# Optimization experiments

Hardware: AMD Instinct MI355X
Metric: run time of the kernel (lower is better)

The kernel has to match this reference:

```python
import jax, jax.numpy as jnp
import numpy as np

SIZES = (20, 20, 20, 20, 20)          # formula_oh_sizes
OH_N = sum(SIZES)                      # 100
NUM_BINS = 65536                       # spect_bin.get_num_bins()
EPS_SIZE = 1e-4                        # eps added to subset size
IN_EPS = 1e-5                          # torch InstanceNorm1d default eps


def thermometer_oh(counts):
    # StructuredOneHot with accum=True: per-element thermometer encoding.
    # counts: (N, E) element counts -> (N, sum(SIZES)) with out[j]=1 iff j < count.
    outs = [(jnp.arange(s, dtype=counts.dtype)[None, :] < counts[:, i:i + 1]).astype(jnp.float32)
            for i, s in enumerate(SIZES)]
    return jnp.concatenate(outs, axis=-1)


def inorm(x):
    # InstanceNorm1d (affine=False) as applied here: normalize over last dim per row.
    m = jnp.mean(x, axis=-1, keepdims=True)
    v = jnp.var(x, axis=-1, keepdims=True)
    return (x - m) * jax.lax.rsqrt(v + IN_EPS)


def _lin(key, fan_in, fan_out):
    k1, k2 = jax.random.split(key)
    bound = 1.0 / np.sqrt(fan_in)
    W = jax.random.uniform(k1, (fan_in, fan_out), jnp.float32, -bound, bound)
    b = jax.random.uniform(k2, (fan_out,), jnp.float32, -bound, bound)
    return W, b


def setup_inputs():
    key = jax.random.key(0)
    ks = jax.random.split(key, 12)
    B, A, GF, S, P, E, D = 8, 48, 256, 4096, 32, 5, 256
    vert_feat_in = jax.random.normal(ks[0], (B, A, GF), jnp.float32)
    vert_mask_in = jnp.ones((B, A), jnp.float32)
    elem_idx = jax.random.randint(ks[1], (B, A), 0, E)
    vert_element_oh = jax.nn.one_hot(elem_idx, E, dtype=jnp.float32)
    adj_oh = jnp.zeros((B, A, A), jnp.float32)                      # unused by forward path
    atom_subsets = jax.random.randint(ks[2], (B, S, A), 0, 2).astype(jnp.int32)
    atom_subsets_peaks = jnp.zeros((1,), jnp.float32)               # unused (mass_idx/intensity used)
    mass_idx = jax.random.randint(ks[3], (B, S, P), 0, NUM_BINS).astype(jnp.int32)
    intensity = jax.random.uniform(ks[4], (B, S, P), jnp.float32)
    combine_W, combine_b = _lin(ks[5], OH_N + GF, GF)
    l1_W, l1_b = _lin(ks[6], GF, D)
    l2a_W, l2a_b = _lin(ks[7], D, D)
    l2b_W, l2b_b = _lin(ks[8], D, D)
    score_W, score_b = _lin(ks[9], D, 1)
    return {
        'vert_feat_in': vert_feat_in, 'vert_mask_in': vert_mask_in,
        'vert_element_oh': vert_element_oh, 'adj_oh': adj_oh,
        'atom_subsets': atom_subsets, 'atom_subsets_peaks': atom_subsets_peaks,
        'mass_idx': mass_idx, 'intensity': intensity,
        'combine_W': combine_W, 'combine_b': combine_b,
        'l1_W': l1_W, 'l1_b': l1_b, 'l2a_W': l2a_W, 'l2a_b': l2a_b,
        'l2b_W': l2b_W, 'l2b_b': l2b_b, 'score_W': score_W, 'score_b': score_b,
    }


def reference(vert_feat_in, vert_mask_in, vert_element_oh, adj_oh, atom_subsets,
              atom_subsets_peaks, mass_idx, intensity,
              combine_W, combine_b, l1_W, l1_b, l2a_W, l2a_b, l2b_W, l2b_b,
              score_W, score_b):
    B, A, GF = vert_feat_in.shape
    _, S, _ = atom_subsets.shape
    subsets_f = atom_subsets.astype(jnp.float32)
    masked_vert = vert_feat_in * vert_mask_in[:, :, None]               # (B,A,GF)
    subsets_masked = subsets_f * vert_mask_in[:, None, :]               # (B,S,A)
    # weighted sum of vertex features over each subset
    sws = jnp.einsum('bag,bsa->bsg', masked_vert, subsets_masked)        # (B,S,GF)
    # per-subset element counts -> structured one-hot formula encoding
    counts = jnp.einsum('bae,bsa->bse', vert_element_oh, subsets_f)      # (B,S,E)
    pf_oh = thermometer_oh(counts.reshape(-1, counts.shape[-1])).reshape(B, S, OH_N)
    subset_size = jnp.sum(subsets_masked, axis=2) + EPS_SIZE             # (B,S)
    mean_feat = sws / subset_size[:, :, None]
    normed = inorm(mean_feat)                                            # subset_weighted_norm
    combined = jax.nn.relu(jnp.concatenate([pf_oh, normed], -1) @ combine_W + combine_b)
    x = inorm(combined)                                                  # norm_post_combine
    x = jax.nn.relu(x @ l1_W + l1_b)
    x = jax.nn.leaky_relu(x @ l2a_W + l2a_b)
    x = jax.nn.leaky_relu(x @ l2b_W + l2b_b)
    x = jax.nn.relu(x)
    x = inorm(x)                                                         # norm_pre_score
    scores = (x @ score_W + score_b)[..., 0]                             # (B,S)
    probs = jax.nn.softmax(scores, axis=-1)
    # per-batch sparse mass-matrix binning: scatter-add intensity*prob into spectral bins
    weighted = intensity * probs[:, :, None]                             # (B,S,P)
    seg = jax.vmap(lambda idx, w: jax.ops.segment_sum(w, idx, num_segments=NUM_BINS))
    spect_out = seg(mass_idx.reshape(B, -1), weighted.reshape(B, -1))    # (B,NUM_BINS)
    return spect_out, probs
```

## Files before the change

### kernel.cpp

```cpp
#include <hip/hip_runtime.h>
#include <math.h>

#define B_DIM 8
#define A_DIM 48
#define GF_DIM 256
#define S_DIM 4096
#define P_DIM 32
#define E_DIM 5
#define OHN 100
#define NBINS 65536
#define XF_STRIDE 268

typedef __attribute__((ext_vector_type(8))) short short8v;
typedef __attribute__((ext_vector_type(4))) float float4v;

__device__ __forceinline__ float wave_sum(float v) {
#pragma unroll
    for (int o = 32; o; o >>= 1) v += __shfl_xor(v, o, 64);
    return v;
}
__device__ __forceinline__ float wave_max(float v) {
#pragma unroll
    for (int o = 32; o; o >>= 1) v = fmaxf(v, __shfl_xor(v, o, 64));
    return v;
}
__device__ __forceinline__ float quad16_sum(float v) {
    v += __shfl_xor(v, 1, 64); v += __shfl_xor(v, 2, 64);
    v += __shfl_xor(v, 4, 64); v += __shfl_xor(v, 8, 64);
    return v;
}
__device__ __forceinline__ unsigned short bf16_rn(float x) {
    unsigned int u = __float_as_uint(x);
    return (unsigned short)((u + 0x7FFFu + ((u >> 16) & 1u)) >> 16);
}
__device__ __forceinline__ float bf16_val(unsigned short h) {
    return __uint_as_float(((unsigned int)h) << 16);
}

__global__ __launch_bounds__(256) void k_wprep(
    const float* __restrict__ cW, const float* __restrict__ l1W,
    const float* __restrict__ l2aW, const float* __restrict__ l2bW,
    short* __restrict__ wp)
{
    int e = blockIdx.x * 256 + threadIdx.x;
    int c = e >> 13;
    int i = e & 8191;
    int j    = i & 7;
    int lane = (i >> 3) & 63;
    int nt   = (i >> 9) & 1;
    int wn   = i >> 10;
    int krel = (lane >> 4) * 8 + j;
    int n    = wn * 32 + nt * 16 + (lane & 15);
    float val = 0.f;
    if (c < 12) {
        int kp = c * 32 + krel;
        if (kp < 100)       val = cW[kp * 256 + n];
        else if (kp >= 128) val = cW[(kp - 28) * 256 + n];
    } else {
        int L  = (c - 12) >> 3;
        int kc = (c - 12) & 7;
        const float* W = (L == 0) ? l1W : (L == 1) ? l2aW : l2bW;
        val = W[(kc * 32 + krel) * 256 + n];
    }
    unsigned short h = bf16_rn(val);
    float lo = val - bf16_val(h);
    int base = c * 16384 + (i & 511);
    wp[base + (wn * 4 + nt) * 512]     = (short)h;
    wp[base + (wn * 4 + 2 + nt) * 512] = (short)bf16_rn(lo);
}

__global__ __launch_bounds__(256) void k_features(
    const float* __restrict__ vert_feat, const float* __restrict__ vert_mask,
    const float* __restrict__ elem_oh, const int* __restrict__ subsets,
    float* __restrict__ x0)
{
    __shared__ float4 vertm[A_DIM][GF_DIM / 4];
    __shared__ float  maskL[A_DIM];
    __shared__ int    eiL[A_DIM];

    const int tid  = threadIdx.x;
    const int lane = tid & 63;
    const int w    = tid >> 6;
    const int b    = blockIdx.x >> 9;
    const int s0   = (blockIdx.x & 511) * 8;

    if (tid < A_DIM) {
        maskL[tid] = vert_mask[b * A_DIM + tid];
        int ei = 0;
#pragma unroll
        for (int e = 0; e < E_DIM; ++e)
            if (elem_oh[(b * A_DIM + tid) * E_DIM + e] > 0.5f) ei = e;
        eiL[tid] = ei;
    }
    __syncthreads();

    const float4* vb = (const float4*)(vert_feat + (size_t)b * A_DIM * GF_DIM);
    for (int idx = tid; idx < A_DIM * (GF_DIM / 4); idx += 256) {
        float4 v = vb[idx];
        float mk = maskL[idx >> 6];
        v.x *= mk; v.y *= mk; v.z *= mk; v.w *= mk;
        vertm[idx >> 6][idx & 63] = v;
    }
    __syncthreads();

    const int   myei   = (lane < A_DIM) ? eiL[lane] : -1;
    const float mymask = (lane < A_DIM) ? maskL[lane] : 0.0f;

#pragma unroll
    for (int i = 0; i < 2; ++i) {
        const int s = s0 + w * 2 + i;
        const int* fp = subsets + ((size_t)b * S_DIM + s) * A_DIM;
        int myflag = (lane < A_DIM) ? fp[lane] : 0;
        float fcoef = (float)myflag * mymask;

        float c0, c1, c2, c3, c4;
        {
            unsigned long long m0 = __ballot(myflag != 0 && myei == 0);
            unsigned long long m1 = __ballot(myflag != 0 && myei == 1);
            unsigned long long m2 = __ballot(myflag != 0 && myei == 2);
            unsigned long long m3 = __ballot(myflag != 0 && myei == 3);
            unsigned long long m4 = __ballot(myflag != 0 && myei == 4);
            c0 = (float)__popcll(m0); c1 = (float)__popcll(m1);
            c2 = (float)__popcll(m2); c3 = (float)__popcll(m3);
            c4 = (float)__popcll(m4);
        }
        float ssize = wave_sum(fcoef) + 1e-4f;

        float4 acc = make_float4(0.f, 0.f, 0.f, 0.f);
        for (int a = 0; a < A_DIM; ++a) {
            float cf = __shfl(fcoef, a, 64);
            float4 vv = vertm[a][lane];
            acc.x = fmaf(cf, vv.x, acc.x);
            acc.y = fmaf(cf, vv.y, acc.y);
            acc.z = fmaf(cf, vv.z, acc.z);
            acc.w = fmaf(cf, vv.w, acc.w);
        }
        float inv = 1.0f / ssize;
        float4 mv = make_float4(acc.x * inv, acc.y * inv, acc.z * inv, acc.w * inv);

        float t = wave_sum(mv.x + mv.y + mv.z + mv.w);
        float m = t * (1.0f / 256.0f);
        float dx = mv.x - m, dy = mv.y - m, dz = mv.z - m, dw = mv.w - m;
        float q = wave_sum(dx * dx + dy * dy + dz * dz + dw * dw);
        float rs = 1.0f / sqrtf(q * (1.0f / 256.0f) + 1e-5f);

        float* xr = x0 + (size_t)(b * S_DIM + s) * XF_STRIDE;
        *(float4*)(xr + lane * 4) = make_float4(dx * rs, dy * rs, dz * rs, dw * rs);
        if (lane < E_DIM)
            xr[256 + lane] = (lane == 0) ? c0 : (lane == 1) ? c1
                           : (lane == 2) ? c2 : (lane == 3) ? c3 : c4;
    }
}

#define OFF_XF  24576
#define OFF_XAL 58880
#define OFF_PS  75264

__device__ __forceinline__ float4v mfma_bf16(short8v a, short8v b, float4v c) {
    return __builtin_amdgcn_mfma_f32_16x16x32_bf16(a, b, c, 0, 0, 0);
}

template <int NKC, int LO0, int ACT, bool NORM, bool SCORE>
__device__ __forceinline__ void layer_pass(
    short* xAh, short* xAl, float (*ps)[32],
    const short* __restrict__ wstream, const float* __restrict__ bias,
    const float* __restrict__ sW, const float* __restrict__ sb,
    float* __restrict__ scores, int R0)
{
    const int tid  = threadIdx.x;
    const int lane = tid & 63;
    const int wn   = tid >> 6;
    const int quad = lane >> 4;
    const int col  = lane & 15;
    const short* wbase = wstream + wn * 2048 + lane * 8;

    float4v acc[2][2];
#pragma unroll
    for (int mi = 0; mi < 2; ++mi)
#pragma unroll
        for (int nt = 0; nt < 2; ++nt) acc[mi][nt] = (float4v){0.f, 0.f, 0.f, 0.f};

    short8v bh[3][2], bl[3][2];
#pragma unroll
    for (int p = 0; p < 2; ++p) {
        if (p < NKC) {
            const short* q = wbase + p * 16384;
            bh[p][0] = *(const short8v*)(q);
            bh[p][1] = *(const short8v*)(q + 512);
            bl[p][0] = *(const short8v*)(q + 1024);
            bl[p][1] = *(const short8v*)(q + 1536);
        }
    }

#pragma unroll
    for (int kc = 0; kc < NKC; ++kc) {
        const int cur = kc % 3;
        if (kc + 2 < NKC) {
            const int nxt = (kc + 2) % 3;
            const short* q = wbase + (kc + 2) * 16384;
            bh[nxt][0] = *(const short8v*)(q);
            bh[nxt][1] = *(const short8v*)(q + 512);
            bl[nxt][0] = *(const short8v*)(q + 1024);
            bl[nxt][1] = *(const short8v*)(q + 1536);
        }
        short8v ah[2], al[2];
#pragma unroll
        for (int mi = 0; mi < 2; ++mi)
            ah[mi] = *(const short8v*)(xAh + ((kc * 2 + mi) * 64 + lane) * 8);
        const bool hlo = (kc >= LO0);
        if (hlo) {
#pragma unroll
            for (int mi = 0; mi < 2; ++mi)
                al[mi] = *(const short8v*)(xAl + (((kc - LO0) * 2 + mi) * 64 + lane) * 8);
        }
#pragma unroll
        for (int mi = 0; mi < 2; ++mi)
#pragma unroll
            for (int nt = 0; nt < 2; ++nt) {
                acc[mi][nt] = mfma_bf16(ah[mi], bh[cur][nt], acc[mi][nt]);
                acc[mi][nt] = mfma_bf16(ah[mi], bl[cur][nt], acc[mi][nt]);
                if (hlo)
                    acc[mi][nt] = mfma_bf16(al[mi], bh[cur][nt], acc[mi][nt]);
            }
    }

    float bc0 = bias[wn * 32 + col];
    float bc1 = bias[wn * 32 + 16 + col];
#pragma unroll
    for (int mi = 0; mi < 2; ++mi)
#pragma unroll
        for (int r = 0; r < 4; ++r) {
            float z0 = acc[mi][0][r] + bc0;
            float z1 = acc[mi][1][r] + bc1;
            if (ACT == 0) { z0 = fmaxf(z0, 0.f); z1 = fmaxf(z1, 0.f); }
            else { z0 = (z0 > 0.f) ? z0 : 0.01f * z0; z1 = (z1 > 0.f) ? z1 : 0.01f * z1; }
            acc[mi][0][r] = z0; acc[mi][1][r] = z1;
        }

    __syncthreads();

    if (NORM) {
        float rsum[2][4];
#pragma unroll
        for (int mi = 0; mi < 2; ++mi)
#pragma unroll
            for (int r = 0; r < 4; ++r)
                rsum[mi][r] = quad16_sum(acc[mi][0][r] + acc[mi][1][r]);
        if (col == 0) {
#pragma unroll
            for (int mi = 0; mi < 2; ++mi)
#pragma unroll
                for (int r = 0; r < 4; ++r)
                    ps[wn][mi * 16 + quad * 4 + r] = rsum[mi][r];
        }
        __syncthreads();
        float mu[2][4];
#pragma unroll
        for (int mi = 0; mi < 2; ++mi)
#pragma unroll
            for (int r = 0; r < 4; ++r) {
                int m = mi * 16 + quad * 4 + r;
                float s = 0.f;
#pragma unroll
                for (int w = 0; w < 8; ++w) s += ps[w][m];
                mu[mi][r] = s * (1.f / 256.f);
            }
        __syncthreads();
        float qs[2][4];
#pragma unroll
        for (int mi = 0; mi < 2; ++mi)
#pragma unroll
            for (int r = 0; r < 4; ++r) {
                acc[mi][0][r] -= mu[mi][r];
                acc[mi][1][r] -= mu[mi][r];
                float q = acc[mi][0][r] * acc[mi][0][r]
                        + acc[mi][1][r] * acc[mi][1][r];
                qs[mi][r] = quad16_sum(q);
            }
        if (col == 0) {
#pragma unroll
            for (int mi = 0; mi < 2; ++mi)
#pragma unroll
                for (int r = 0; r < 4; ++r)
                    ps[wn][mi * 16 + quad * 4 + r] = qs[mi][r];
        }
        __syncthreads();
#pragma unroll
        for (int mi = 0; mi < 2; ++mi)
#pragma unroll
            for (int r = 0; r < 4; ++r) {
                int m = mi * 16 + quad * 4 + r;
                float s = 0.f;
#pragma unroll
                for (int w = 0; w < 8; ++w) s += ps[w][m];
                float rsf = 1.0f / sqrtf(s * (1.f / 256.f) + 1e-5f);
                acc[mi][0][r] *= rsf;
                acc[mi][1][r] *= rsf;
            }
    }

    if (SCORE) {
        __syncthreads();
        float sv0 = sW[wn * 32 + col];
        float sv1 = sW[wn * 32 + 16 + col];
        float psu[2][4];
#pragma unroll
        for (int mi = 0; mi < 2; ++mi)
#pragma unroll
            for (int r = 0; r < 4; ++r)
                psu[mi][r] = quad16_sum(acc[mi][0][r] * sv0 + acc[mi][1][r] * sv1);
        if (col == 0) {
#pragma unroll
            for (int mi = 0; mi < 2; ++mi)
#pragma unroll
                for (int r = 0; r < 4; ++r)
                    ps[wn][mi * 16 + quad * 4 + r] = psu[mi][r];
        }
        __syncthreads();
        if (tid < 32) {
            float s = sb[0];
#pragma unroll
            for (int w = 0; w < 8; ++w) s += ps[w][tid];
            scores[R0 + tid] = s;
        }
    } else {
#pragma unroll
        for (int mi = 0; mi < 2; ++mi)
#pragma unroll
            for (int nt = 0; nt < 2; ++nt) {
                int nn0 = (nt * 16 + col) & ~1;
                int q2  = nn0 >> 3;
                int j0  = nn0 & 7;
#pragma unroll
                for (int r = 0; r < 4; ++r) {
                    float v  = acc[mi][nt][r];
                    float pv = __shfl_xor(v, 1, 64);
                    int m15 = quad * 4 + r;
                    int rowidx = (wn * 2 + mi) * 64 + q2 * 16 + m15;
                    if ((col & 1) == 0) {
                        unsigned int wd = (unsigned int)bf16_rn(v)
                                        | ((unsigned int)bf16_rn(pv) << 16);
                        ((unsigned int*)xAh)[rowidx * 4 + (j0 >> 1)] = wd;
                    } else {
                        float ls = v  - bf16_val(bf16_rn(v));
                        float lp = pv - bf16_val(bf16_rn(pv));
                        unsigned int wd = (unsigned int)bf16_rn(lp)
                                        | ((unsigned int)bf16_rn(ls) << 16);
                        ((unsigned int*)xAl)[rowidx * 4 + (j0 >> 1)] = wd;
                    }
                }
            }
        __syncthreads();
    }
}

__global__ __launch_bounds__(512, 4) void k_mlp(
    const float* __restrict__ x0, const short* __restrict__ wprep,
    const float* __restrict__ cb,  const float* __restrict__ l1b,
    const float* __restrict__ l2ab, const float* __restrict__ l2bb,
    const float* __restrict__ sW,  const float* __restrict__ sb,
    float* __restrict__ scores)
{
    __shared__ __align__(16) char smem[76288];
    short*  xAh = (short*)smem;
    float*  xf  = (float*)(smem + OFF_XF);
    short*  xAl = (short*)(smem + OFF_XAL);
    float (*ps)[32] = (float(*)[32])(smem + OFF_PS);

    const int tid = threadIdx.x;
    const int fb  = blockIdx.x;
    const int R0  = fb * 32;

    {
        const float4* src = (const float4*)(x0 + (size_t)fb * 32 * XF_STRIDE);
        for (int i = tid; i < 2144; i += 512) ((float4*)xf)[i] = src[i];
    }
    __syncthreads();

    {
#pragma unroll
        for (int g0 = 0; g0 < 3; ++g0) {
            int g  = tid + g0 * 512;
            int lt = g & 63;
            int t2 = g >> 6;
            int kc = t2 >> 1, mi = t2 & 1;
            int m  = mi * 16 + (lt & 15);
            int kb = (lt >> 4) * 8;
            if (kc < 4) {
                float c[5];
#pragma unroll
                for (int e = 0; e < 5; ++e) c[e] = xf[m * XF_STRIDE + 256 + e];
                short8v hv;
#pragma unroll
                for (int j = 0; j < 8; ++j) {
                    int kp = kc * 32 + kb + j;
                    float val = 0.f;
                    if (kp < 100) {
                        int e = kp / 20;
                        val = ((float)(kp - e * 20) < c[e]) ? 1.0f : 0.0f;
                    }
                    hv[j] = (short)bf16_rn(val);
                }
                *(short8v*)(xAh + g * 8) = hv;
            } else {
                const float* srcp = xf + m * XF_STRIDE + (kc - 4) * 32 + kb;
                float4 f0 = *(const float4*)(srcp);
                float4 f1 = *(const float4*)(srcp + 4);
                float fv[8] = {f0.x, f0.y, f0.z, f0.w, f1.x, f1.y, f1.z, f1.w};
                short8v hv, lv;
#pragma unroll
                for (int j = 0; j < 8; ++j) {
                    unsigned short h = bf16_rn(fv[j]);
                    hv[j] = (short)h;
                    lv[j] = (short)bf16_rn(fv[j] - bf16_val(h));
                }
                *(short8v*)(xAh + g * 8) = hv;
                *(short8v*)(xAl + (g - 512) * 8) = lv;
            }
        }
    }
    __syncthreads();

    layer_pass<12, 4, 0, true,  false>(xAh, xAl, ps, wprep,
        cb, nullptr, nullptr, nullptr, R0);
    layer_pass< 8, 0, 0, false, false>(xAh, xAl, ps, wprep + 12 * 16384,
        l1b, nullptr, nullptr, nullptr, R0);
    layer_pass< 8, 0, 1, false, false>(xAh, xAl, ps, wprep + 20 * 16384,
        l2ab, nullptr, nullptr, nullptr, R0);
    layer_pass< 8, 0, 0, true,  true >(xAh, xAl, ps, wprep + 28 * 16384,
        l2bb, sW, sb, scores, R0);
}

__global__ __launch_bounds__(256) void k_softmax(float* __restrict__ probs) {
    const int b   = blockIdx.x;
    const int tid = threadIdx.x;
    __shared__ float redA[4];
    __shared__ float redB[4];
    float* sp = probs + (size_t)b * S_DIM;

    float v[16];
    float mx = -INFINITY;
#pragma unroll
    for (int i = 0; i < 16; ++i) {
        v[i] = sp[tid + i * 256];
        mx = fmaxf(mx, v[i]);
    }
    mx = wave_max(mx);
    if ((tid & 63) == 0) redA[tid >> 6] = mx;
    __syncthreads();
    mx = fmaxf(fmaxf(redA[0], redA[1]), fmaxf(redA[2], redA[3]));

    float sum = 0.f;
#pragma unroll
    for (int i = 0; i < 16; ++i) {
        v[i] = expf(v[i] - mx);
        sum += v[i];
    }
    sum = wave_sum(sum);
    if ((tid & 63) == 0) redB[tid >> 6] = sum;
    __syncthreads();
    float tot = redB[0] + redB[1] + redB[2] + redB[3];
    float inv = 1.0f / tot;
#pragma unroll
    for (int i = 0; i < 16; ++i) sp[tid + i * 256] = v[i] * inv;
}

__global__ __launch_bounds__(256) void k_zero4(float4* __restrict__ p, int n4) {
    int i = blockIdx.x * 256 + threadIdx.x;
    if (i < n4) p[i] = make_float4(0.f, 0.f, 0.f, 0.f);
}

__global__ __launch_bounds__(256) void k_scatter(
    const int*   __restrict__ mass_idx,
    const float* __restrict__ intensity,
    const float* __restrict__ probs,
    float* __restrict__ spect)
{
    int i  = blockIdx.x * 256 + threadIdx.x;
    int bs = i >> 5;
    int b  = i >> 17;
    float w = intensity[i] * probs[bs];
    unsafeAtomicAdd(spect + ((size_t)b << 16) + mass_idx[i], w);
}

extern "C" void kernel_launch(void* const* d_in, const int* in_sizes, int n_in,
                              void* d_out, int out_size, void* d_ws, size_t ws_size,
                              hipStream_t stream) {
    const float* vert_feat = (const float*)d_in[0];
    const float* vert_mask = (const float*)d_in[1];
    const float* elem_oh   = (const float*)d_in[2];
    const int*   subsets   = (const int*)d_in[4];
    const int*   mass_idx  = (const int*)d_in[6];
    const float* intensity = (const float*)d_in[7];
    const float* combine_W = (const float*)d_in[8];
    const float* combine_b = (const float*)d_in[9];
    const float* l1_W      = (const float*)d_in[10];
    const float* l1_b      = (const float*)d_in[11];
    const float* l2a_W     = (const float*)d_in[12];
    const float* l2a_b     = (const float*)d_in[13];
    const float* l2b_W     = (const float*)d_in[14];
    const float* l2b_b     = (const float*)d_in[15];
    const float* score_W   = (const float*)d_in[16];
    const float* score_b   = (const float*)d_in[17];

    float* out   = (float*)d_out;
    float* spect = out;
    float* probs = out + (size_t)B_DIM * NBINS;

    short* wprep = (short*)d_ws;
    float* x0    = (float*)(wprep + 36 * 16384);

    k_wprep<<<1152, 256, 0, stream>>>(combine_W, l1_W, l2a_W, l2b_W, wprep);
    k_features<<<4096, 256, 0, stream>>>(vert_feat, vert_mask, elem_oh, subsets, x0);
    k_mlp<<<1024, 512, 0, stream>>>(x0, wprep,
        combine_b, l1_b, l2a_b, l2b_b, score_W, score_b, probs);
    k_softmax<<<B_DIM, 256, 0, stream>>>(probs);
    k_zero4<<<(B_DIM * NBINS / 4) / 256, 256, 0, stream>>>(
        (float4*)spect, B_DIM * NBINS / 4);
    k_scatter<<<(B_DIM * S_DIM * P_DIM) / 256, 256, 0, stream>>>(
        mass_idx, intensity, probs, spect);
}
```

Baseline: 284.6 us.

## Fuse subset feature aggregation into MLP kernel via MFMA against prepped vertex features

Removes the separate k_features kernel and the x0 intermediate buffer. The subset-weighted feature sum is now computed inside k_mlp as a bf16 hi/lo MFMA of the subset mask matrix against masked vertex features, which a merged prep kernel lays out per batch. Element counts and inverse subset sizes are computed per block in LDS, and LDS use shrinks, so launch bounds are raised to 6 blocks per CU. This cuts a kernel launch and the global round trip of the feature matrix, but splits the fp32 vertex features into bf16 hi and lo parts, which may shift precision slightly.

```diff
diff --git a/kernel.cpp b/kernel.cpp
--- a/kernel.cpp
+++ b/kernel.cpp
@@ -9,7 +9,6 @@
 #define E_DIM 5
 #define OHN 100
 #define NBINS 65536
-#define XF_STRIDE 268
 
 typedef __attribute__((ext_vector_type(8))) short short8v;
 typedef __attribute__((ext_vector_type(4))) float float4v;
@@ -36,129 +35,85 @@
 __device__ __forceinline__ float bf16_val(unsigned short h) {
     return __uint_as_float(((unsigned int)h) << 16);
 }
-
-__global__ __launch_bounds__(256) void k_wprep(
+__device__ __forceinline__ float4v mfma_bf16(short8v a, short8v b, float4v c) {
+    return __builtin_amdgcn_mfma_f32_16x16x32_bf16(a, b, c, 0, 0, 0);
+}
+
+__global__ __launch_bounds__(256) void k_prep(
     const float* __restrict__ cW, const float* __restrict__ l1W,
     const float* __restrict__ l2aW, const float* __restrict__ l2bW,
-    short* __restrict__ wp)
+    const float* __restrict__ vert_feat, const float* __restrict__ vert_mask,
+    const float* __restrict__ elem_oh,
+    short* __restrict__ wp, short* __restrict__ wv,
+    float* __restrict__ maskB, int* __restrict__ eiB)
 {
-    int e = blockIdx.x * 256 + threadIdx.x;
-    int c = e >> 13;
-    int i = e & 8191;
-    int j    = i & 7;
-    int lane = (i >> 3) & 63;
-    int nt   = (i >> 9) & 1;
-    int wn   = i >> 10;
-    int krel = (lane >> 4) * 8 + j;
-    int n    = wn * 32 + nt * 16 + (lane & 15);
-    float val = 0.f;
-    if (c < 12) {
-        int kp = c * 32 + krel;
-        if (kp < 100)       val = cW[kp * 256 + n];
-        else if (kp >= 128) val = cW[(kp - 28) * 256 + n];
+    const int blk = blockIdx.x;
+    const int tid = threadIdx.x;
+    if (blk < 1152) {
+        int e = blk * 256 + tid;
+        int c = e >> 13;
+        int i = e & 8191;
+        int j    = i & 7;
+        int lane = (i >> 3) & 63;
+        int nt   = (i >> 9) & 1;
+        int wn   = i >> 10;
+        int krel = (lane >> 4) * 8 + j;
+        int n    = wn * 32 + nt * 16 + (lane & 15);
+        float val = 0.f;
+        if (c < 12) {
+            int kp = c * 32 + krel;
+            if (kp < 100)       val = cW[kp * 256 + n];
+            else if (kp >= 128) val = cW[(kp - 28) * 256 + n];
+        } else {
+            int L  = (c - 12) >> 3;
+            int kc = (c - 12) & 7;
+            const float* W = (L == 0) ? l1W : (L == 1) ? l2aW : l2bW;
+            val = W[(kc * 32 + krel) * 256 + n];
+        }
+        unsigned short h = bf16_rn(val);
+        float lo = val - bf16_val(h);
+        int base = c * 16384 + (i & 511);
+        wp[base + (wn * 4 + nt) * 512]     = (short)h;
+        wp[base + (wn * 4 + 2 + nt) * 512] = (short)bf16_rn(lo);
+    } else if (blk < 1664) {
+        int vb = blk - 1152;
+        int vc = vb >> 5;
+        int i  = (vb & 31) * 256 + tid;
+        int b  = vc >> 1, v = vc & 1;
+        int j    = i & 7;
+        int lane = (i >> 3) & 63;
+        int nt   = (i >> 9) & 1;
+        int wn   = i >> 10;
+        int k = v * 32 + (lane >> 4) * 8 + j;
+        int n = wn * 32 + nt * 16 + (lane & 15);
+        float val = 0.f;
+        if (k < A_DIM) {
+            float mk = vert_mask[b * A_DIM + k];
+            val = vert_feat[((size_t)(b * A_DIM + k)) * GF_DIM + n] * mk * mk;
+        }
+        unsigned short h = bf16_rn(val);
+        float lo = val - bf16_val(h);
+        int base = vc * 16384 + (i & 511);
+        wv[base + (wn * 4 + nt) * 512]     = (short)h;
+        wv[base + (wn * 4 + 2 + nt) * 512] = (short)bf16_rn(lo);
     } else {
-        int L  = (c - 12) >> 3;
-        int kc = (c - 12) & 7;
-        const float* W = (L == 0) ? l1W : (L == 1) ? l2aW : l2bW;
-        val = W[(kc * 32 + krel) * 256 + n];
-    }
-    unsigned short h = bf16_rn(val);
-    float lo = val - bf16_val(h);
-    int base = c * 16384 + (i & 511);
-    wp[base + (wn * 4 + nt) * 512]     = (short)h;
-    wp[base + (wn * 4 + 2 + nt) * 512] = (short)bf16_rn(lo);
-}
-
-__global__ __launch_bounds__(256) void k_features(
-    const float* __restrict__ vert_feat, const float* __restrict__ vert_mask,
-    const float* __restrict__ elem_oh, const int* __restrict__ subsets,
-    float* __restrict__ x0)
-{
-    __shared__ float4 vertm[A_DIM][GF_DIM / 4];
-    __shared__ float  maskL[A_DIM];
-    __shared__ int    eiL[A_DIM];
-
-    const int tid  = threadIdx.x;
-    const int lane = tid & 63;
-    const int w    = tid >> 6;
-    const int b    = blockIdx.x >> 9;
-    const int s0   = (blockIdx.x & 511) * 8;
-
-    if (tid < A_DIM) {
-        maskL[tid] = vert_mask[b * A_DIM + tid];
-        int ei = 0;
-#pragma unroll
-        for (int e = 0; e < E_DIM; ++e)
-            if (elem_oh[(b * A_DIM + tid) * E_DIM + e] > 0.5f) ei = e;
-        eiL[tid] = ei;
-    }
-    __syncthreads();
-
-    const float4* vb = (const float4*)(vert_feat + (size_t)b * A_DIM * GF_DIM);
-    for (int idx = tid; idx < A_DIM * (GF_DIM / 4); idx += 256) {
-        float4 v = vb[idx];
-        float mk = maskL[idx >> 6];
-        v.x *= mk; v.y *= mk; v.z *= mk; v.w *= mk;
-        vertm[idx >> 6][idx & 63] = v;
-    }
-    __syncthreads();
-
-    const int   myei   = (lane < A_DIM) ? eiL[lane] : -1;
-    const float mymask = (lane < A_DIM) ? maskL[lane] : 0.0f;
-
-#pragma unroll
-    for (int i = 0; i < 2; ++i) {
-        const int s = s0 + w * 2 + i;
-        const int* fp = subsets + ((size_t)b * S_DIM + s) * A_DIM;
-        int myflag = (lane < A_DIM) ? fp[lane] : 0;
-        float fcoef = (float)myflag * mymask;
-
-        float c0, c1, c2, c3, c4;
-        {
-            unsigned long long m0 = __ballot(myflag != 0 && myei == 0);
-            unsigned long long m1 = __ballot(myflag != 0 && myei == 1);
-            unsigned long long m2 = __ballot(myflag != 0 && myei == 2);
-            unsigned long long m3 = __ballot(myflag != 0 && myei == 3);
-            unsigned long long m4 = __ballot(myflag != 0 && myei == 4);
-            c0 = (float)__popcll(m0); c1 = (float)__popcll(m1);
-            c2 = (float)__popcll(m2); c3 = (float)__popcll(m3);
-            c4 = (float)__popcll(m4);
-        }
-        float ssize = wave_sum(fcoef) + 1e-4f;
-
-        float4 acc = make_float4(0.f, 0.f, 0.f, 0.f);
-        for (int a = 0; a < A_DIM; ++a) {
-            float cf = __shfl(fcoef, a, 64);
-            float4 vv = vertm[a][lane];
-            acc.x = fmaf(cf, vv.x, acc.x);
-            acc.y = fmaf(cf, vv.y, acc.y);
-            acc.z = fmaf(cf, vv.z, acc.z);
-            acc.w = fmaf(cf, vv.w, acc.w);
-        }
-        float inv = 1.0f / ssize;
-        float4 mv = make_float4(acc.x * inv, acc.y * inv, acc.z * inv, acc.w * inv);
-
-        float t = wave_sum(mv.x + mv.y + mv.z + mv.w);
-        float m = t * (1.0f / 256.0f);
-        float dx = mv.x - m, dy = mv.y - m, dz = mv.z - m, dw = mv.w - m;
-        float q = wave_sum(dx * dx + dy * dy + dz * dz + dw * dw);
-        float rs = 1.0f / sqrtf(q * (1.0f / 256.0f) + 1e-5f);
-
-        float* xr = x0 + (size_t)(b * S_DIM + s) * XF_STRIDE;
-        *(float4*)(xr + lane * 4) = make_float4(dx * rs, dy * rs, dz * rs, dw * rs);
-        if (lane < E_DIM)
-            xr[256 + lane] = (lane == 0) ? c0 : (lane == 1) ? c1
-                           : (lane == 2) ? c2 : (lane == 3) ? c3 : c4;
-    }
-}
-
-#define OFF_XF  24576
-#define OFF_XAL 58880
-#define OFF_PS  75264
-
-__device__ __forceinline__ float4v mfma_bf16(short8v a, short8v b, float4v c) {
-    return __builtin_amdgcn_mfma_f32_16x16x32_bf16(a, b, c, 0, 0, 0);
-}
+        for (int t = tid; t < B_DIM * A_DIM; t += 256) {
+            maskB[t] = vert_mask[t];
+            int ei = 0;
+#pragma unroll
+            for (int e = 0; e < E_DIM; ++e)
+                if (elem_oh[t * E_DIM + e] > 0.5f) ei = e;
+            eiB[t] = ei;
+        }
+    }
+}
+
+#define L_XAL 24576
+#define L_FM  40960
+#define L_PS  45056
+#define L_CNT 46080
+#define L_INV 46720
+#define L_TOT 46848
 
 template <int NKC, int LO0, int ACT, bool NORM, bool SCORE>
 __device__ __forceinline__ void layer_pass(
@@ -354,72 +309,229 @@
     }
 }
 
-__global__ __launch_bounds__(512, 4) void k_mlp(
-    const float* __restrict__ x0, const short* __restrict__ wprep,
+__global__ __launch_bounds__(512, 6) void k_mlp(
+    const int* __restrict__ subsets, const short* __restrict__ wprep,
+    const short* __restrict__ vertB,
+    const float* __restrict__ maskB, const int* __restrict__ eiB,
     const float* __restrict__ cb,  const float* __restrict__ l1b,
     const float* __restrict__ l2ab, const float* __restrict__ l2bb,
     const float* __restrict__ sW,  const float* __restrict__ sb,
     float* __restrict__ scores)
 {
-    __shared__ __align__(16) char smem[76288];
+    __shared__ __align__(16) char smem[L_TOT];
     short*  xAh = (short*)smem;
-    float*  xf  = (float*)(smem + OFF_XF);
-    short*  xAl = (short*)(smem + OFF_XAL);
-    float (*ps)[32] = (float(*)[32])(smem + OFF_PS);
-
-    const int tid = threadIdx.x;
-    const int fb  = blockIdx.x;
-    const int R0  = fb * 32;
+    short*  xAl = (short*)(smem + L_XAL);
+    short*  fm  = (short*)(smem + L_FM);
+    float (*ps)[32]  = (float(*)[32])(smem + L_PS);
+    float (*cnt)[5]  = (float(*)[5])(smem + L_CNT);
+    float*  invsz    = (float*)(smem + L_INV);
+
+    const int tid  = threadIdx.x;
+    const int lane = tid & 63;
+    const int wn   = tid >> 6;
+    const int quad = lane >> 4;
+    const int col  = lane & 15;
+    const int fb   = blockIdx.x;
+    const int b    = fb >> 7;
+    const int R0   = fb * 32;
+
+    if (tid < 256) {
+        int g  = tid;
+        int lg = g & 63;
+        int t2 = g >> 6;
+        int kc = t2 >> 1, mi = t2 & 1;
+        int m  = mi * 16 + (lg & 15);
+        int k0 = kc * 32 + (lg >> 4) * 8;
+        const int* srow = subsets + (size_t)(R0 + m) * A_DIM;
+        short8v hv;
+#pragma unroll
+        for (int j = 0; j < 8; ++j) {
+            int k = k0 + j;
+            hv[j] = (short)((k < A_DIM && srow[k]) ? 0x3F80 : 0);
+        }
+        *(short8v*)(fm + g * 8) = hv;
+    }
 
     {
-        const float4* src = (const float4*)(x0 + (size_t)fb * 32 * XF_STRIDE);
-        for (int i = tid; i < 2144; i += 512) ((float4*)xf)[i] = src[i];
+        const float mymask = (lane < A_DIM) ? maskB[b * A_DIM + lane] : 0.f;
+        const int   myei   = (lane < A_DIM) ? eiB[b * A_DIM + lane]   : -1;
+#pragma unroll
+        for (int i = 0; i < 4; ++i) {
+            int r = wn * 4 + i;
+            int fl = (lane < A_DIM) ? subsets[(size_t)(R0 + r) * A_DIM + lane] : 0;
+            unsigned long long m0 = __ballot(fl != 0 && myei == 0);
+            unsigned long long m1 = __ballot(fl != 0 && myei == 1);
+            unsigned long long m2 = __ballot(fl != 0 && myei == 2);
+            unsigned long long m3 = __ballot(fl != 0 && myei == 3);
+            unsigned long long m4 = __ballot(fl != 0 && myei == 4);
+            float ssz = wave_sum(fl ? mymask : 0.f) + 1e-4f;
+            if (lane == 0) {
+                cnt[r][0] = (float)__popcll(m0);
+                cnt[r][1] = (float)__popcll(m1);
+                cnt[r][2] = (float)__popcll(m2);
+                cnt[r][3] = (float)__popcll(m3);
+                cnt[r][4] = (float)__popcll(m4);
+                invsz[r]  = 1.0f / ssz;
+            }
+        }
     }
     __syncthreads();
 
     {
-#pragma unroll
-        for (int g0 = 0; g0 < 3; ++g0) {
-            int g  = tid + g0 * 512;
-            int lt = g & 63;
+        const short* wbase = vertB + b * 32768 + wn * 2048 + lane * 8;
+        float4v acc[2][2];
+#pragma unroll
+        for (int mi = 0; mi < 2; ++mi)
+#pragma unroll
+            for (int nt = 0; nt < 2; ++nt) acc[mi][nt] = (float4v){0.f, 0.f, 0.f, 0.f};
+
+        short8v bh[2][2], bl[2][2];
+#pragma unroll
+        for (int kc = 0; kc < 2; ++kc) {
+            const short* q = wbase + kc * 16384;
+            bh[kc][0] = *(const short8v*)(q);
+            bh[kc][1] = *(const short8v*)(q + 512);
+            bl[kc][0] = *(const short8v*)(q + 1024);
+            bl[kc][1] = *(const short8v*)(q + 1536);
+        }
+#pragma unroll
+        for (int kc = 0; kc < 2; ++kc) {
+            short8v a0 = *(const short8v*)(fm + ((kc * 2 + 0) * 64 + lane) * 8);
+            short8v a1 = *(const short8v*)(fm + ((kc * 2 + 1) * 64 + lane) * 8);
+#pragma unroll
+            for (int nt = 0; nt < 2; ++nt) {
+                acc[0][nt] = mfma_bf16(a0, bh[kc][nt], acc[0][nt]);
+                acc[0][nt] = mfma_bf16(a0, bl[kc][nt], acc[0][nt]);
+                acc[1][nt] = mfma_bf16(a1, bh[kc][nt], acc[1][nt]);
+                acc[1][nt] = mfma_bf16(a1, bl[kc][nt], acc[1][nt]);
+            }
+        }
+
+#pragma unroll
+        for (int mi = 0; mi < 2; ++mi)
+#pragma unroll
+            for (int r = 0; r < 4; ++r) {
+                float iv = invsz[mi * 16 + quad * 4 + r];
+                acc[mi][0][r] *= iv;
+                acc[mi][1][r] *= iv;
+            }
+
+        __syncthreads();
+
+        {
+            float rsum[2][4];
+#pragma unroll
+            for (int mi = 0; mi < 2; ++mi)
+#pragma unroll
+                for (int r = 0; r < 4; ++r)
+                    rsum[mi][r] = quad16_sum(acc[mi][0][r] + acc[mi][1][r]);
+            if (col == 0) {
+#pragma unroll
+                for (int mi = 0; mi < 2; ++mi)
+#pragma unroll
+                    for (int r = 0; r < 4; ++r)
+                        ps[wn][mi * 16 + quad * 4 + r] = rsum[mi][r];
+            }
+            __syncthreads();
+            float mu[2][4];
+#pragma unroll
+            for (int mi = 0; mi < 2; ++mi)
+#pragma unroll
+                for (int r = 0; r < 4; ++r) {
+                    int m = mi * 16 + quad * 4 + r;
+                    float s = 0.f;
+#pragma unroll
+                    for (int w = 0; w < 8; ++w) s += ps[w][m];
+                    mu[mi][r] = s * (1.f / 256.f);
+                }
+            __syncthreads();
+            float qs[2][4];
+#pragma unroll
+            for (int mi = 0; mi < 2; ++mi)
+#pragma unroll
+                for (int r = 0; r < 4; ++r) {
+                    acc[mi][0][r] -= mu[mi][r];
+                    acc[mi][1][r] -= mu[mi][r];
+                    float q = acc[mi][0][r] * acc[mi][0][r]
+                            + acc[mi][1][r] * acc[mi][1][r];
+                    qs[mi][r] = quad16_sum(q);
+                }
+            if (col == 0) {
+#pragma unroll
+                for (int mi = 0; mi < 2; ++mi)
+#pragma unroll
+                    for (int r = 0; r < 4; ++r)
+                        ps[wn][mi * 16 + quad * 4 + r] = qs[mi][r];
+            }
+            __syncthreads();
+#pragma unroll
+            for (int mi = 0; mi < 2; ++mi)
+#pragma unroll
+                for (int r = 0; r < 4; ++r) {
+                    int m = mi * 16 + quad * 4 + r;
+                    float s = 0.f;
+#pragma unroll
+                    for (int w = 0; w < 8; ++w) s += ps[w][m];
+                    float rsf = 1.0f / sqrtf(s * (1.f / 256.f) + 1e-5f);
+                    acc[mi][0][r] *= rsf;
+                    acc[mi][1][r] *= rsf;
+                }
+        }
+
+#pragma unroll
+        for (int mi = 0; mi < 2; ++mi)
+#pragma unroll
+            for (int nt = 0; nt < 2; ++nt) {
+                int nn0 = (nt * 16 + col) & ~1;
+                int q2  = nn0 >> 3;
+                int j0  = nn0 & 7;
+#pragma unroll
+                for (int r = 0; r < 4; ++r) {
+                    float v  = acc[mi][nt][r];
+                    float pv = __shfl_xor(v, 1, 64);
+                    int m15 = quad * 4 + r;
+                    int rh = ((4 + wn) * 2 + mi) * 64 + q2 * 16 + m15;
+                    int rl = (wn * 2 + mi) * 64 + q2 * 16 + m15;
+                    if ((col & 1) == 0) {
+                        unsigned int wd = (unsigned int)bf16_rn(v)
+                                        | ((unsigned int)bf16_rn(pv) << 16);
+                        ((unsigned int*)xAh)[rh * 4 + (j0 >> 1)] = wd;
+                    } else {
+                        float ls = v  - bf16_val(bf16_rn(v));
+                        float lp = pv - bf16_val(bf16_rn(pv));
+                        unsigned int wd = (unsigned int)bf16_rn(lp)
+                                        | ((unsigned int)bf16_rn(ls) << 16);
+                        ((unsigned int*)xAl)[rl * 4 + (j0 >> 1)] = wd;
+                    }
+                }
+            }
+
+        {
+            int g  = tid;
+            int lg = g & 63;
             int t2 = g >> 6;
             int kc = t2 >> 1, mi = t2 & 1;
-            int m  = mi * 16 + (lt & 15);
-            int kb = (lt >> 4) * 8;
-            if (kc < 4) {
-                float c[5];
-#pragma unroll
-                for (int e = 0; e < 5; ++e) c[e] = xf[m * XF_STRIDE + 256 + e];
-                short8v hv;
-#pragma unroll
-                for (int j = 0; j < 8; ++j) {
-                    int kp = kc * 32 + kb + j;
-                    float val = 0.f;
-                    if (kp < 100) {
-                        int e = kp / 20;
-                        val = ((float)(kp - e * 20) < c[e]) ? 1.0f : 0.0f;
-                    }
-                    hv[j] = (short)bf16_rn(val);
+            int m  = mi * 16 + (lg & 15);
+            int kb = (lg >> 4) * 8;
+            float c0 = cnt[m][0], c1 = cnt[m][1], c2 = cnt[m][2],
+                  c3 = cnt[m][3], c4 = cnt[m][4];
+            short8v hv;
+#pragma unroll
+            for (int j = 0; j < 8; ++j) {
+                int kp = kc * 32 + kb + j;
+                float val = 0.f;
+                if (kp < 100) {
+                    int e = kp / 20;
+                    float ce = (e == 0) ? c0 : (e == 1) ? c1 : (e == 2) ? c2
+                             : (e == 3) ? c3 : c4;
+                    val = ((float)(kp - e * 20) < ce) ? 1.0f : 0.0f;
                 }
-                *(short8v*)(xAh + g * 8) = hv;
-            } else {
-                const float* srcp = xf + m * XF_STRIDE + (kc - 4) * 32 + kb;
-                float4 f0 = *(const float4*)(srcp);
-                float4 f1 = *(const float4*)(srcp + 4);
-                float fv[8] = {f0.x, f0.y, f0.z, f0.w, f1.x, f1.y, f1.z, f1.w};
-                short8v hv, lv;
-#pragma unroll
-                for (int j = 0; j < 8; ++j) {
-                    unsigned short h = bf16_rn(fv[j]);
-                    hv[j] = (short)h;
-                    lv[j] = (short)bf16_rn(fv[j] - bf16_val(h));
-                }
-                *(short8v*)(xAh + g * 8) = hv;
-                *(short8v*)(xAl + (g - 512) * 8) = lv;
-            }
-        }
-    }
-    __syncthreads();
+                hv[j] = (short)((val != 0.f) ? 0x3F80 : 0);
+            }
+            *(short8v*)(xAh + g * 8) = hv;
+        }
+        __syncthreads();
+    }
 
     layer_pass<12, 4, 0, true,  false>(xAh, xAl, ps, wprep,
         cb, nullptr, nullptr, nullptr, R0);
@@ -508,11 +620,13 @@
     float* probs = out + (size_t)B_DIM * NBINS;
 
     short* wprep = (short*)d_ws;
-    float* x0    = (float*)(wprep + 36 * 16384);
-
-    k_wprep<<<1152, 256, 0, stream>>>(combine_W, l1_W, l2a_W, l2b_W, wprep);
-    k_features<<<4096, 256, 0, stream>>>(vert_feat, vert_mask, elem_oh, subsets, x0);
-    k_mlp<<<1024, 512, 0, stream>>>(x0, wprep,
+    short* vertB = wprep + 36 * 16384;
+    float* maskB = (float*)(vertB + 16 * 16384);
+    int*   eiB   = (int*)(maskB + B_DIM * A_DIM);
+
+    k_prep<<<1665, 256, 0, stream>>>(combine_W, l1_W, l2a_W, l2b_W,
+        vert_feat, vert_mask, elem_oh, wprep, vertB, maskB, eiB);
+    k_mlp<<<1024, 512, 0, stream>>>(subsets, wprep, vertB, maskB, eiB,
         combine_b, l1_b, l2a_b, l2b_b, score_W, score_b, probs);
     k_softmax<<<B_DIM, 256, 0, stream>>>(probs);
     k_zero4<<<(B_DIM * NBINS / 4) / 256, 256, 0, stream>>>(
```

Result: faster. 266.2 us (-6.5%).
